# Performance work log

Measured on AMD Instinct MI355X. Metric: run time of the kernel, lower is better.

The kernel has to match this reference:

```python
import jax, jax.numpy as jnp
import numpy as np

B, S, D = 4, 2048, 256
H = 8
HD = D // H
FF = 1024
LEN_M1 = 513


def _layer_norm(x, gamma, beta, eps=1e-5):
    m = jnp.mean(x, axis=-1, keepdims=True)
    v = jnp.var(x, axis=-1, keepdims=True)
    return (x - m) * jax.lax.rsqrt(v + eps) * gamma + beta


def setup_inputs() -> dict:
    key = jax.random.key(0)
    ks = jax.random.split(key, 16)
    s = 0.02  # init scale for weights
    return {
        "src": jax.random.normal(ks[0], (B, S, D), dtype=jnp.float32),
        "Wq": jax.random.normal(ks[1], (D, D), dtype=jnp.float32) * s,
        "bq": jnp.zeros((D,), dtype=jnp.float32),
        "Wk": jax.random.normal(ks[2], (D, D), dtype=jnp.float32) * s,
        "bk": jnp.zeros((D,), dtype=jnp.float32),
        "Wv": jax.random.normal(ks[3], (D, D), dtype=jnp.float32) * s,
        "bv": jnp.zeros((D,), dtype=jnp.float32),
        "Wo": jax.random.normal(ks[4], (D, D), dtype=jnp.float32) * s,
        "bo": jnp.zeros((D,), dtype=jnp.float32),
        "W1": jax.random.normal(ks[5], (FF, D), dtype=jnp.float32) * s,
        "b1": jnp.zeros((FF,), dtype=jnp.float32),
        "W2": jax.random.normal(ks[6], (D, FF), dtype=jnp.float32) * s,
        "b2": jnp.zeros((D,), dtype=jnp.float32),
        "g1": jnp.ones((D,), dtype=jnp.float32),
        "be1": jnp.zeros((D,), dtype=jnp.float32),
        "g2": jnp.ones((D,), dtype=jnp.float32),
        "be2": jnp.zeros((D,), dtype=jnp.float32),
        "len_m1": LEN_M1,
    }


def reference(src, Wq, bq, Wk, bk, Wv, bv, Wo, bo, W1, b1, W2, b2, g1, be1, g2, be2, len_m1):
    Bb, Ss, Dd = src.shape
    hd = Dd // H
    # projections (torch Linear: x @ W.T + b), split heads -> [B,H,S,hd]
    q = (src @ Wq.T + bq).reshape(Bb, Ss, H, hd).transpose(0, 2, 1, 3)
    k = (src @ Wk.T + bk).reshape(Bb, Ss, H, hd).transpose(0, 2, 1, 3)
    v = (src @ Wv.T + bv).reshape(Bb, Ss, H, hd).transpose(0, 2, 1, 3)
    scores = jnp.einsum("bhqd,bhkd->bhqk", q, k) / np.sqrt(hd).astype(np.float32)
    # causal mask + global prefix block: masked where j > i OR (i < len_m1 and j >= len_m1)
    i = jnp.arange(Ss)[:, None]
    j = jnp.arange(Ss)[None, :]
    mask = (j > i) | ((i < len_m1) & (j >= len_m1))
    scores = jnp.where(mask, -jnp.inf, scores)
    attn = jax.nn.softmax(scores, axis=-1)
    ao = jnp.einsum("bhqk,bhkd->bhqd", attn, v).transpose(0, 2, 1, 3).reshape(Bb, Ss, Dd)
    src2 = _layer_norm(src + (ao @ Wo.T + bo), g1, be1)
    ff = jax.nn.gelu(src2 @ W1.T + b1, approximate=False) @ W2.T + b2
    return _layer_norm(src2 + ff, g2, be2)
```

## Files before the change

### kernel.cpp

```cpp
#include <hip/hip_runtime.h>
#include <math.h>

#define NB 4
#define NS 2048
#define ND 256
#define NH 8
#define NHD 32
#define NFF 1024
#define NM (NB*NS)
#define KPAD 40
#define VSP 72
#define VTP 72
#define AS 264
#define QSCALE 0.2550181657f

typedef __attribute__((ext_vector_type(4))) short short4v;
typedef __attribute__((ext_vector_type(8))) short short8v;
typedef __attribute__((ext_vector_type(4))) float f32x4;
typedef unsigned short us;

__device__ __forceinline__ us f2bf(float f){
  union { float f; unsigned u; } c; c.f = f;
  unsigned u = c.u + 0x7fffu + ((c.u >> 16) & 1u);
  return (us)(u >> 16);
}

__global__ __launch_bounds__(256) void prep_kernel(
    const float* __restrict__ src,
    const float* __restrict__ Wq, const float* __restrict__ Wk, const float* __restrict__ Wv,
    const float* __restrict__ Wo, const float* __restrict__ W1, const float* __restrict__ W2,
    const float* __restrict__ bq,
    us* __restrict__ X, us* __restrict__ Wqkvb, us* __restrict__ Wob,
    us* __restrict__ W1b, us* __restrict__ W2b, float* __restrict__ bqs){
  unsigned bid = blockIdx.x;
  if (bid == 1408){ bqs[threadIdx.x] = bq[threadIdx.x]*QSCALE; return; }
  unsigned u = bid*256u + threadIdx.x;
  const float* sp; us* dp; float sc = 1.f;
  if (u < 262144u){ sp = src + (size_t)u*8; dp = X + (size_t)u*8; }
  else {
    unsigned v = u - 262144u;
    if      (v <  8192u){ sp = Wq + (size_t)v*8;            dp = Wqkvb + (size_t)v*8;            sc = QSCALE; }
    else if (v < 16384u){ sp = Wk + (size_t)(v- 8192u)*8;   dp = Wqkvb + 65536 + (size_t)(v- 8192u)*8; }
    else if (v < 24576u){ sp = Wv + (size_t)(v-16384u)*8;   dp = Wqkvb + 131072 + (size_t)(v-16384u)*8; }
    else if (v < 32768u){ sp = Wo + (size_t)(v-24576u)*8;   dp = Wob + (size_t)(v-24576u)*8; }
    else if (v < 65536u){ sp = W1 + (size_t)(v-32768u)*8;   dp = W1b + (size_t)(v-32768u)*8; }
    else               { sp = W2 + (size_t)(v-65536u)*8;    dp = W2b + (size_t)(v-65536u)*8; }
  }
  float4 a = *(const float4*)sp, b = *(const float4*)(sp+4);
  short8v o;
  o[0]=(short)f2bf(a.x*sc); o[1]=(short)f2bf(a.y*sc); o[2]=(short)f2bf(a.z*sc); o[3]=(short)f2bf(a.w*sc);
  o[4]=(short)f2bf(b.x*sc); o[5]=(short)f2bf(b.y*sc); o[6]=(short)f2bf(b.z*sc); o[7]=(short)f2bf(b.w*sc);
  *(short8v*)dp = o;
}

template<int KTOT, int EPI>
__global__ __launch_bounds__(256) void gemm_kernel(
    const us* __restrict__ A, const us* __restrict__ W,
    const float* __restrict__ bias0, const float* __restrict__ bias1, const float* __restrict__ bias2,
    us* __restrict__ outb, us* __restrict__ outv){
  __shared__ us Asl[64*AS];
  const int t = threadIdx.x, l = t&63, wv = t>>6;
  const int lx = l&15, lw = l>>4;
  const int m0 = blockIdx.y*64;
  const int n0 = blockIdx.x*128 + wv*32;

  f32x4 acc[4][2];
  #pragma unroll
  for(int mb=0;mb<4;mb++)
    #pragma unroll
    for(int nb=0;nb<2;nb++) acc[mb][nb] = (f32x4){0.f,0.f,0.f,0.f};

  for (int kc = 0; kc < KTOT; kc += 256){
    __syncthreads();
    #pragma unroll
    for (int it=0; it<8; it++){
      int idx = it*256 + t;
      int r = idx>>5, c = idx&31;
      *(short8v*)&Asl[r*AS + c*8] = *(const short8v*)(A + (size_t)(m0+r)*KTOT + kc + c*8);
    }
    __syncthreads();
    short8v bf[2][8];
    #pragma unroll
    for (int nb=0; nb<2; nb++)
      #pragma unroll
      for (int ks=0; ks<8; ks++)
        bf[nb][ks] = *(const short8v*)(W + (size_t)(n0 + nb*16 + lx)*KTOT + kc + ks*32 + 8*lw);
    #pragma unroll
    for (int ks=0; ks<8; ks++){
      short8v af[4];
      #pragma unroll
      for (int mb=0; mb<4; mb++)
        af[mb] = *(const short8v*)&Asl[(mb*16+lx)*AS + ks*32 + 8*lw];
      #pragma unroll
      for (int mb=0; mb<4; mb++){
        acc[mb][0] = __builtin_amdgcn_mfma_f32_16x16x32_bf16(af[mb], bf[0][ks], acc[mb][0], 0,0,0);
        acc[mb][1] = __builtin_amdgcn_mfma_f32_16x16x32_bf16(af[mb], bf[1][ks], acc[mb][1], 0,0,0);
      }
    }
  }
  const int mr0 = m0 + 4*lw;
  #pragma unroll
  for (int nb=0; nb<2; nb++){
    int n = n0 + nb*16 + lx;
    if (EPI == 0){
      int seg = n >> 8, nn = n & 255;
      const float* bp = (seg==0) ? bias0 : (seg==1) ? bias1 : bias2;
      float bb = bp[nn];
      if (seg < 2){
        us* op = outb + (size_t)seg*((size_t)NM*ND) + nn;
        #pragma unroll
        for (int mb=0; mb<4; mb++)
          #pragma unroll
          for (int r=0; r<4; r++)
            op[(size_t)(mr0 + mb*16 + r)*ND] = f2bf(acc[mb][nb][r] + bb);
      } else {
        int hh = nn >> 5, dd = nn & 31;
        int bidx = mr0 >> 11;
        int s0 = mr0 & 2047;
        us* vp = outv + (((size_t)bidx*NH + hh)*NHD + dd)*NS;
        #pragma unroll
        for (int mb=0; mb<4; mb++){
          short4v v4;
          #pragma unroll
          for (int r=0; r<4; r++) v4[r] = (short)f2bf(acc[mb][nb][r] + bb);
          *(short4v*)(vp + s0 + mb*16) = v4;
        }
      }
    } else {
      float bb = bias0[n];
      #pragma unroll
      for (int mb=0; mb<4; mb++)
        #pragma unroll
        for (int r=0; r<4; r++){
          float x = acc[mb][nb][r] + bb;
          float g = 0.5f*x*(1.f + erff(x*0.70710678118654752f));
          outb[(size_t)(mr0 + mb*16 + r)*NFF + n] = f2bf(g);
        }
    }
  }
}

template<int KTOT, bool WRITE_BF16>
__global__ __launch_bounds__(256) void gemm_ln_kernel(
    const us* __restrict__ A, const us* __restrict__ W,
    const float* __restrict__ bias, const float* __restrict__ resid,
    const float* __restrict__ g, const float* __restrict__ be,
    us* __restrict__ outb, float* __restrict__ outf){
  __shared__ us Asl[32*AS];
  __shared__ float red[4][32][2];
  const int t = threadIdx.x, l = t&63, wv = t>>6;
  const int lx = l&15, lw = l>>4;
  const int m0 = blockIdx.x*32;
  const int n0 = wv*64;

  f32x4 acc[2][4];
  #pragma unroll
  for(int mb=0;mb<2;mb++)
    #pragma unroll
    for(int nb=0;nb<4;nb++) acc[mb][nb] = (f32x4){0.f,0.f,0.f,0.f};

  for (int kc = 0; kc < KTOT; kc += 256){
    __syncthreads();
    #pragma unroll
    for (int it=0; it<4; it++){
      int idx = it*256 + t;
      int r = idx>>5, c = idx&31;
      *(short8v*)&Asl[r*AS + c*8] = *(const short8v*)(A + (size_t)(m0+r)*KTOT + kc + c*8);
    }
    __syncthreads();
    #pragma unroll
    for (int ks=0; ks<8; ks++){
      short8v af[2];
      #pragma unroll
      for (int mb=0; mb<2; mb++)
        af[mb] = *(const short8v*)&Asl[(mb*16+lx)*AS + ks*32 + 8*lw];
      #pragma unroll
      for (int nb=0; nb<4; nb++){
        short8v bfv = *(const short8v*)(W + (size_t)(n0 + nb*16 + lx)*KTOT + kc + ks*32 + 8*lw);
        acc[0][nb] = __builtin_amdgcn_mfma_f32_16x16x32_bf16(af[0], bfv, acc[0][nb], 0,0,0);
        acc[1][nb] = __builtin_amdgcn_mfma_f32_16x16x32_bf16(af[1], bfv, acc[1][nb], 0,0,0);
      }
    }
  }
  #pragma unroll
  for (int nb=0; nb<4; nb++){
    int n = n0 + nb*16 + lx;
    float bb = bias[n];
    #pragma unroll
    for (int mb=0; mb<2; mb++)
      #pragma unroll
      for (int r=0; r<4; r++){
        int m = m0 + mb*16 + 4*lw + r;
        acc[mb][nb][r] += bb + resid[(size_t)m*ND + n];
      }
  }
  float ps[2][4], pq[2][4];
  #pragma unroll
  for (int mb=0; mb<2; mb++)
    #pragma unroll
    for (int r=0; r<4; r++){
      float s = acc[mb][0][r] + acc[mb][1][r] + acc[mb][2][r] + acc[mb][3][r];
      float q = acc[mb][0][r]*acc[mb][0][r] + acc[mb][1][r]*acc[mb][1][r]
              + acc[mb][2][r]*acc[mb][2][r] + acc[mb][3][r]*acc[mb][3][r];
      ps[mb][r] = s; pq[mb][r] = q;
    }
  #pragma unroll
  for (int o=1; o<16; o<<=1){
    #pragma unroll
    for (int mb=0; mb<2; mb++)
      #pragma unroll
      for (int r=0; r<4; r++){
        ps[mb][r] += __shfl_xor(ps[mb][r], o);
        pq[mb][r] += __shfl_xor(pq[mb][r], o);
      }
  }
  if (lx == 0){
    #pragma unroll
    for (int mb=0; mb<2; mb++)
      #pragma unroll
      for (int r=0; r<4; r++){
        red[wv][mb*16 + 4*lw + r][0] = ps[mb][r];
        red[wv][mb*16 + 4*lw + r][1] = pq[mb][r];
      }
  }
  __syncthreads();
  float mean_[2][4], rstd_[2][4];
  #pragma unroll
  for (int mb=0; mb<2; mb++)
    #pragma unroll
    for (int r=0; r<4; r++){
      int ml = mb*16 + 4*lw + r;
      float s = red[0][ml][0] + red[1][ml][0] + red[2][ml][0] + red[3][ml][0];
      float q = red[0][ml][1] + red[1][ml][1] + red[2][ml][1] + red[3][ml][1];
      float mean = s*(1.f/ND);
      float var = q*(1.f/ND) - mean*mean;
      mean_[mb][r] = mean;
      rstd_[mb][r] = rsqrtf(var + 1e-5f);
    }
  #pragma unroll
  for (int nb=0; nb<4; nb++){
    int n = n0 + nb*16 + lx;
    float gv = g[n], bev = be[n];
    #pragma unroll
    for (int mb=0; mb<2; mb++)
      #pragma unroll
      for (int r=0; r<4; r++){
        int m = m0 + mb*16 + 4*lw + r;
        float y = (acc[mb][nb][r] - mean_[mb][r])*rstd_[mb][r]*gv + bev;
        if (WRITE_BF16) outb[(size_t)m*ND + n] = f2bf(y);
        outf[(size_t)m*ND + n] = y;
      }
  }
}

template<bool MASK>
__device__ __forceinline__ void attn_tile(
    const us* __restrict__ Kl, const us* __restrict__ Vl, us* __restrict__ pw,
    const short8v qf, const int lx, const int lw, const int jt, const int qg,
    f32x4& acc0, f32x4& acc1, float& lsum){
  f32x4 s4[4];
  #pragma unroll
  for (int kb=0; kb<4; kb++){
    short8v kf = *(const short8v*)(Kl + (kb*16 + lx)*KPAD + 8*lw);
    f32x4 z = {0.f,0.f,0.f,0.f};
    s4[kb] = __builtin_amdgcn_mfma_f32_16x16x32_bf16(kf, qf, z, 0,0,0);
  }
  float p[16];
  #pragma unroll
  for (int kb=0; kb<4; kb++)
    #pragma unroll
    for (int r=0; r<4; r++){
      float x = exp2f(s4[kb][r]);
      if (MASK) x = ((jt + 16*kb + 4*lw + r) > qg) ? 0.f : x;
      p[kb*4+r] = x;
      lsum += x;
    }
  #pragma unroll
  for (int kb=0; kb<4; kb++){
    unsigned p0, p1;
    asm("v_cvt_pk_bf16_f32 %0, %1, %2" : "=v"(p0) : "v"(p[4*kb+0]), "v"(p[4*kb+1]));
    asm("v_cvt_pk_bf16_f32 %0, %1, %2" : "=v"(p1) : "v"(p[4*kb+2]), "v"(p[4*kb+3]));
    uint2 pk; pk.x = p0; pk.y = p1;
    *(uint2*)(pw + (size_t)lx*VTP + kb*16 + 4*lw) = pk;
  }
  #pragma unroll
  for (int c=0; c<2; c++){
    short8v pf  = *(const short8v*)(pw + (size_t)lx*VTP + 32*c + 8*lw);
    short8v vfL = *(const short8v*)(Vl + (size_t)( lx    )*VSP + 32*c + 8*lw);
    short8v vfH = *(const short8v*)(Vl + (size_t)(16+lx  )*VSP + 32*c + 8*lw);
    acc0 = __builtin_amdgcn_mfma_f32_16x16x32_bf16(vfL, pf, acc0, 0,0,0);
    acc1 = __builtin_amdgcn_mfma_f32_16x16x32_bf16(vfH, pf, acc1, 0,0,0);
  }
}

__global__ __launch_bounds__(256) void attn_kernel(
    const us* __restrict__ Q, const us* __restrict__ K,
    const us* __restrict__ Vt, us* __restrict__ AO){
  __shared__ us Klds[2][64*KPAD];
  __shared__ us Vs[2][32*VSP];
  __shared__ us Ex[4][16*VTP];

  const int t = threadIdx.x, l = t & 63, wv = t >> 6;
  const int lx = l & 15, lw = l >> 4;
  const int bid = blockIdx.x;
  const int qtile = 31 - (bid >> 5);
  const int bh = bid & 31;
  const int b = bh >> 3, h = bh & 7;
  const int qbase = qtile*64 + wv*16;
  const int qg = qbase + lx;

  const us* Qg = Q + ((size_t)b*NS)*ND + h*NHD;
  const us* Kg = K + ((size_t)b*NS)*ND + h*NHD;
  const us* Vg = Vt + (size_t)bh*NHD*NS;

  short8v qf = *(const short8v*)(Qg + (size_t)(qbase + lx)*ND + 8*lw);

  f32x4 acc0 = {0.f,0.f,0.f,0.f}, acc1 = {0.f,0.f,0.f,0.f};
  float lsum = 0.f;

  const int kr = t >> 2, kp = t & 3;
  const int vd = t >> 3, vp = t & 7;
  const int jmax = qtile*64;
  us* pw = &Ex[wv][0];

  {
    short8v k0 = *(const short8v*)(Kg + (size_t)kr*ND + kp*8);
    short8v v0 = *(const short8v*)(Vg + (size_t)vd*NS + vp*8);
    *(short8v*)&Klds[0][kr*KPAD + kp*8] = k0;
    *(short8v*)&Vs[0][vd*VSP + vp*8] = v0;
  }
  __syncthreads();

  int cur = 0;
  for (int jt = 0; jt < jmax; jt += 64){
    short8v kn = *(const short8v*)(Kg + (size_t)(jt + 64 + kr)*ND + kp*8);
    short8v vn = *(const short8v*)(Vg + (size_t)vd*NS + (jt + 64) + vp*8);
    attn_tile<false>(&Klds[cur][0], &Vs[cur][0], pw, qf, lx, lw, jt, qg, acc0, acc1, lsum);
    *(short8v*)&Klds[cur^1][kr*KPAD + kp*8] = kn;
    *(short8v*)&Vs[cur^1][vd*VSP + vp*8] = vn;
    __syncthreads();
    cur ^= 1;
  }
  attn_tile<true>(&Klds[cur][0], &Vs[cur][0], pw, qf, lx, lw, jmax, qg, acc0, acc1, lsum);

  float lt = lsum + __shfl_xor(lsum, 16);
  lt += __shfl_xor(lt, 32);
  float inv = 1.f / lt;
  float* ol = (float*)&Ex[wv][0];
  #pragma unroll
  for (int r=0;r<4;r++){
    ol[lx*36 +      4*lw + r] = acc0[r]*inv;
    ol[lx*36 + 16 + 4*lw + r] = acc1[r]*inv;
  }
  int rr = l >> 2, cc = l & 3;
  const float* op8 = &ol[rr*36 + cc*8];
  short8v o8;
  #pragma unroll
  for (int j=0;j<8;j++) o8[j] = (short)f2bf(op8[j]);
  *(short8v*)(AO + ((size_t)(b*NS + qbase + rr))*ND + h*NHD + cc*8) = o8;
}

extern "C" void kernel_launch(void* const* d_in, const int* in_sizes, int n_in,
                              void* d_out, int out_size, void* d_ws, size_t ws_size,
                              hipStream_t stream){
  const float* src = (const float*)d_in[0];
  const float* Wq  = (const float*)d_in[1];
  const float* bq  = (const float*)d_in[2];
  const float* Wk  = (const float*)d_in[3];
  const float* bk  = (const float*)d_in[4];
  const float* Wv  = (const float*)d_in[5];
  const float* bv  = (const float*)d_in[6];
  const float* Wo  = (const float*)d_in[7];
  const float* bo  = (const float*)d_in[8];
  const float* W1  = (const float*)d_in[9];
  const float* b1  = (const float*)d_in[10];
  const float* W2  = (const float*)d_in[11];
  const float* b2  = (const float*)d_in[12];
  const float* g1  = (const float*)d_in[13];
  const float* be1 = (const float*)d_in[14];
  const float* g2  = (const float*)d_in[15];
  const float* be2 = (const float*)d_in[16];

  const size_t MB = 1048576;
  unsigned char* w8 = (unsigned char*)d_ws;
  us* X     = (us*)(w8 + 0);
  us* Qb    = (us*)(w8 + 4*MB);
  us* Kb    = (us*)(w8 + 8*MB);
  us* Vtg   = (us*)(w8 + 12*MB);
  us* AO    = (us*)(w8 + 16*MB);
  us* S2b   = (us*)(w8 + 20*MB);
  us* FF    = (us*)(w8 + 24*MB);
  us* Wqkvb = (us*)(w8 + 40*MB);
  us* Wob   = (us*)(w8 + 40*MB + 384*1024);
  us* W1b   = (us*)(w8 + 40*MB + 512*1024);
  us* W2b   = (us*)(w8 + 40*MB + 1024*1024);
  float* bqs = (float*)(w8 + 40*MB + 1536*1024);
  float* S2f = (float*)(w8 + 42*MB);
  float* out = (float*)d_out;

  prep_kernel<<<1409, 256, 0, stream>>>(src, Wq,Wk,Wv,Wo,W1,W2, bq,
                                        X, Wqkvb, Wob, W1b, W2b, bqs);
  gemm_kernel<256,0><<<dim3(6,128), 256, 0, stream>>>(X, Wqkvb, bqs, bk, bv, Qb, Vtg);
  attn_kernel<<<1024, 256, 0, stream>>>(Qb, Kb, Vtg, AO);
  gemm_ln_kernel<256,true><<<256, 256, 0, stream>>>(AO, Wob, bo, src, g1, be1, S2b, S2f);
  gemm_kernel<256,2><<<dim3(8,128), 256, 0, stream>>>(S2b, W1b, b1, nullptr, nullptr, FF, nullptr);
  gemm_ln_kernel<1024,false><<<256, 256, 0, stream>>>(FF, W2b, b2, S2f, g2, be2, nullptr, out);
}
```

Baseline: 119.4 us.

## Halve GEMM+LayerNorm row tile and double-buffer A tiles in LDS

The fused GEMM+LayerNorm kernel now processes 16 rows per block instead of 32, doubling the grid from 256 to 512 blocks so more of the GPU's compute units are occupied. The A operand uses two LDS buffers: the next K chunk is loaded into registers while MFMAs run on the current chunk, which removes one barrier per iteration. Weight fragments are loaded in a batch before the MFMAs. In exchange, each weight fragment is reused across half as many rows, so total weight reads from cache roughly double.

New measurement: 116.2 us. -2.7%, faster.

```diff
diff --git a/kernel.cpp b/kernel.cpp
--- a/kernel.cpp
+++ b/kernel.cpp
@@ -146,40 +146,53 @@
     const float* __restrict__ bias, const float* __restrict__ resid,
     const float* __restrict__ g, const float* __restrict__ be,
     us* __restrict__ outb, float* __restrict__ outf){
-  __shared__ us Asl[32*AS];
-  __shared__ float red[4][32][2];
+  __shared__ us Asl[2][16*AS];
+  __shared__ float red[4][16][2];
   const int t = threadIdx.x, l = t&63, wv = t>>6;
   const int lx = l&15, lw = l>>4;
-  const int m0 = blockIdx.x*32;
+  const int m0 = blockIdx.x*16;
   const int n0 = wv*64;
 
-  f32x4 acc[2][4];
-  #pragma unroll
-  for(int mb=0;mb<2;mb++)
-    #pragma unroll
-    for(int nb=0;nb<4;nb++) acc[mb][nb] = (f32x4){0.f,0.f,0.f,0.f};
-
+  f32x4 acc[4];
+  #pragma unroll
+  for(int nb=0;nb<4;nb++) acc[nb] = (f32x4){0.f,0.f,0.f,0.f};
+
+  #pragma unroll
+  for (int it=0; it<2; it++){
+    int idx = it*256 + t, r = idx>>5, c = idx&31;
+    *(short8v*)&Asl[0][r*AS + c*8] = *(const short8v*)(A + (size_t)(m0+r)*KTOT + c*8);
+  }
+  __syncthreads();
+  int cur = 0;
   for (int kc = 0; kc < KTOT; kc += 256){
-    __syncthreads();
-    #pragma unroll
-    for (int it=0; it<4; it++){
-      int idx = it*256 + t;
-      int r = idx>>5, c = idx&31;
-      *(short8v*)&Asl[r*AS + c*8] = *(const short8v*)(A + (size_t)(m0+r)*KTOT + kc + c*8);
-    }
-    __syncthreads();
+    short8v an[2];
+    const bool more = (kc + 256) < KTOT;
+    if (more){
+      #pragma unroll
+      for (int it=0; it<2; it++){
+        int idx = it*256 + t, r = idx>>5, c = idx&31;
+        an[it] = *(const short8v*)(A + (size_t)(m0+r)*KTOT + kc + 256 + c*8);
+      }
+    }
     #pragma unroll
     for (int ks=0; ks<8; ks++){
-      short8v af[2];
-      #pragma unroll
-      for (int mb=0; mb<2; mb++)
-        af[mb] = *(const short8v*)&Asl[(mb*16+lx)*AS + ks*32 + 8*lw];
-      #pragma unroll
-      for (int nb=0; nb<4; nb++){
-        short8v bfv = *(const short8v*)(W + (size_t)(n0 + nb*16 + lx)*KTOT + kc + ks*32 + 8*lw);
-        acc[0][nb] = __builtin_amdgcn_mfma_f32_16x16x32_bf16(af[0], bfv, acc[0][nb], 0,0,0);
-        acc[1][nb] = __builtin_amdgcn_mfma_f32_16x16x32_bf16(af[1], bfv, acc[1][nb], 0,0,0);
+      short8v bfv[4];
+      #pragma unroll
+      for (int nb=0; nb<4; nb++)
+        bfv[nb] = *(const short8v*)(W + (size_t)(n0 + nb*16 + lx)*KTOT + kc + ks*32 + 8*lw);
+      short8v af = *(const short8v*)&Asl[cur][lx*AS + ks*32 + 8*lw];
+      #pragma unroll
+      for (int nb=0; nb<4; nb++)
+        acc[nb] = __builtin_amdgcn_mfma_f32_16x16x32_bf16(af, bfv[nb], acc[nb], 0,0,0);
+    }
+    if (more){
+      #pragma unroll
+      for (int it=0; it<2; it++){
+        int idx = it*256 + t, r = idx>>5, c = idx&31;
+        *(short8v*)&Asl[cur^1][r*AS + c*8] = an[it];
       }
+      __syncthreads();
+      cur ^= 1;
     }
   }
   #pragma unroll
@@ -187,69 +200,47 @@
     int n = n0 + nb*16 + lx;
     float bb = bias[n];
     #pragma unroll
-    for (int mb=0; mb<2; mb++)
-      #pragma unroll
-      for (int r=0; r<4; r++){
-        int m = m0 + mb*16 + 4*lw + r;
-        acc[mb][nb][r] += bb + resid[(size_t)m*ND + n];
-      }
-  }
-  float ps[2][4], pq[2][4];
-  #pragma unroll
-  for (int mb=0; mb<2; mb++)
-    #pragma unroll
     for (int r=0; r<4; r++){
-      float s = acc[mb][0][r] + acc[mb][1][r] + acc[mb][2][r] + acc[mb][3][r];
-      float q = acc[mb][0][r]*acc[mb][0][r] + acc[mb][1][r]*acc[mb][1][r]
-              + acc[mb][2][r]*acc[mb][2][r] + acc[mb][3][r]*acc[mb][3][r];
-      ps[mb][r] = s; pq[mb][r] = q;
-    }
-  #pragma unroll
-  for (int o=1; o<16; o<<=1){
-    #pragma unroll
-    for (int mb=0; mb<2; mb++)
-      #pragma unroll
-      for (int r=0; r<4; r++){
-        ps[mb][r] += __shfl_xor(ps[mb][r], o);
-        pq[mb][r] += __shfl_xor(pq[mb][r], o);
-      }
-  }
-  if (lx == 0){
-    #pragma unroll
-    for (int mb=0; mb<2; mb++)
-      #pragma unroll
-      for (int r=0; r<4; r++){
-        red[wv][mb*16 + 4*lw + r][0] = ps[mb][r];
-        red[wv][mb*16 + 4*lw + r][1] = pq[mb][r];
-      }
-  }
+      int m = m0 + 4*lw + r;
+      acc[nb][r] += bb + resid[(size_t)m*ND + n];
+    }
+  }
+  float ps[4], pq[4];
+  #pragma unroll
+  for (int r=0; r<4; r++){
+    ps[r] = acc[0][r]+acc[1][r]+acc[2][r]+acc[3][r];
+    pq[r] = acc[0][r]*acc[0][r]+acc[1][r]*acc[1][r]+acc[2][r]*acc[2][r]+acc[3][r]*acc[3][r];
+  }
+  #pragma unroll
+  for (int o=1; o<16; o<<=1)
+    #pragma unroll
+    for (int r=0; r<4; r++){ ps[r] += __shfl_xor(ps[r], o); pq[r] += __shfl_xor(pq[r], o); }
+  if (lx == 0)
+    #pragma unroll
+    for (int r=0; r<4; r++){ red[wv][4*lw+r][0] = ps[r]; red[wv][4*lw+r][1] = pq[r]; }
   __syncthreads();
-  float mean_[2][4], rstd_[2][4];
-  #pragma unroll
-  for (int mb=0; mb<2; mb++)
-    #pragma unroll
-    for (int r=0; r<4; r++){
-      int ml = mb*16 + 4*lw + r;
-      float s = red[0][ml][0] + red[1][ml][0] + red[2][ml][0] + red[3][ml][0];
-      float q = red[0][ml][1] + red[1][ml][1] + red[2][ml][1] + red[3][ml][1];
-      float mean = s*(1.f/ND);
-      float var = q*(1.f/ND) - mean*mean;
-      mean_[mb][r] = mean;
-      rstd_[mb][r] = rsqrtf(var + 1e-5f);
-    }
+  float mean_[4], rstd_[4];
+  #pragma unroll
+  for (int r=0; r<4; r++){
+    int ml = 4*lw + r;
+    float s = red[0][ml][0]+red[1][ml][0]+red[2][ml][0]+red[3][ml][0];
+    float q = red[0][ml][1]+red[1][ml][1]+red[2][ml][1]+red[3][ml][1];
+    float mean = s*(1.f/ND);
+    float var = q*(1.f/ND) - mean*mean;
+    mean_[r] = mean;
+    rstd_[r] = rsqrtf(var + 1e-5f);
+  }
   #pragma unroll
   for (int nb=0; nb<4; nb++){
     int n = n0 + nb*16 + lx;
     float gv = g[n], bev = be[n];
     #pragma unroll
-    for (int mb=0; mb<2; mb++)
-      #pragma unroll
-      for (int r=0; r<4; r++){
-        int m = m0 + mb*16 + 4*lw + r;
-        float y = (acc[mb][nb][r] - mean_[mb][r])*rstd_[mb][r]*gv + bev;
-        if (WRITE_BF16) outb[(size_t)m*ND + n] = f2bf(y);
-        outf[(size_t)m*ND + n] = y;
-      }
+    for (int r=0; r<4; r++){
+      int m = m0 + 4*lw + r;
+      float y = (acc[nb][r] - mean_[r])*rstd_[r]*gv + bev;
+      if (WRITE_BF16) outb[(size_t)m*ND + n] = f2bf(y);
+      outf[(size_t)m*ND + n] = y;
+    }
   }
 }
 
@@ -402,7 +393,7 @@
                                         X, Wqkvb, Wob, W1b, W2b, bqs);
   gemm_kernel<256,0><<<dim3(6,128), 256, 0, stream>>>(X, Wqkvb, bqs, bk, bv, Qb, Vtg);
   attn_kernel<<<1024, 256, 0, stream>>>(Qb, Kb, Vtg, AO);
-  gemm_ln_kernel<256,true><<<256, 256, 0, stream>>>(AO, Wob, bo, src, g1, be1, S2b, S2f);
+  gemm_ln_kernel<256,true><<<512, 256, 0, stream>>>(AO, Wob, bo, src, g1, be1, S2b, S2f);
   gemm_kernel<256,2><<<dim3(8,128), 256, 0, stream>>>(S2b, W1b, b1, nullptr, nullptr, FF, nullptr);
-  gemm_ln_kernel<1024,false><<<256, 256, 0, stream>>>(FF, W2b, b2, S2f, g2, be2, nullptr, out);
-}
+  gemm_ln_kernel<1024,false><<<512, 256, 0, stream>>>(FF, W2b, b2, S2f, g2, be2, nullptr, out);
+}
```
